# Optimization experiments

Hardware: AMD Instinct MI355X
Metric: run time of the kernel (lower is better)

The kernel has to match this reference:

```python
import jax, jax.numpy as jnp
import numpy as np

N_NODES = 100000
N_EDGES = 1600000
D_IN = 128
D_HID = 128
SCALE = 1.8
EPS = 1e-12


def setup_inputs() -> dict:
    key = jax.random.key(0)
    ks = jax.random.split(key, 7)
    x = jax.random.normal(ks[0], (N_NODES, D_IN), dtype=jnp.float32)
    W1 = jax.random.normal(ks[1], (D_HID, D_IN), dtype=jnp.float32) * 0.05
    b1 = jax.random.normal(ks[2], (D_HID,), dtype=jnp.float32) * 0.05
    W2 = jax.random.normal(ks[3], (D_HID, D_HID), dtype=jnp.float32) * 0.05
    b2 = jax.random.normal(ks[4], (D_HID,), dtype=jnp.float32) * 0.05
    src = jax.random.randint(ks[5], (N_EDGES,), 0, N_NODES, dtype=jnp.int64 if jax.config.jax_enable_x64 else jnp.int32)
    dst = jax.random.randint(ks[6], (N_EDGES,), 0, N_NODES, dtype=jnp.int64 if jax.config.jax_enable_x64 else jnp.int32)
    return {"x": x, "W1": W1, "b1": b1, "W2": W2, "b2": b2, "src": src, "dst": dst}


def reference(x, W1, b1, W2, b2, src, dst):
    N = x.shape[0]
    ones = jnp.ones((src.shape[0],), dtype=x.dtype)
    # GraphConv norm='both' degree normalizers (clamped to >=1 as in DGL)
    deg_out = jnp.maximum(jnp.zeros((N,), x.dtype).at[src].add(ones), 1.0)
    deg_in = jnp.maximum(jnp.zeros((N,), x.dtype).at[dst].add(ones), 1.0)
    norm_out = jax.lax.rsqrt(deg_out)[:, None]  # [N,1]
    norm_in = jax.lax.rsqrt(deg_in)[:, None]    # [N,1]

    def layer(h, W, b):
        # torch.nn.Linear: h @ W.T + b
        h = jnp.einsum('nd,kd->nk', h, W) + b
        # F.normalize(h, dim=1) * 1.8
        nrm = jnp.sqrt(jnp.sum(h * h, axis=1, keepdims=True))
        h = h / jnp.maximum(nrm, EPS) * SCALE
        # GraphConv (weight=False, bias=False, norm='both'):
        # D_out^{-1/2} -> sparse aggregate -> D_in^{-1/2}
        h = h * norm_out
        agg = jax.ops.segment_sum(h[src], dst, num_segments=N)
        return agg * norm_in

    h = layer(x, W1, b1)
    h = layer(h, W2, b2)
    return h
```

## Files before the change

kernel.cpp:

```cpp
#include <hip/hip_runtime.h>
#include <cstdint>
#include <cstddef>

#define D 128
#define NSCALE 1.8f
#define NEPS 1e-12f
#define EPB 8192
#define NLO 512
#define SCAP 9216
#define SRCB 23
#define SRCM 0x7FFFFF

typedef __attribute__((ext_vector_type(8))) short bf16x8;
typedef __attribute__((ext_vector_type(4))) float f32x4;

__device__ __forceinline__ ushort bf16_rtn(float f) {
    uint32_t u = __float_as_uint(f);
    u = u + 0x7FFFu + ((u >> 16) & 1u);
    return (ushort)(u >> 16);
}

__device__ __forceinline__ float blo(uint32_t u) { return __uint_as_float(u << 16); }
__device__ __forceinline__ float bhi(uint32_t u) { return __uint_as_float(u & 0xFFFF0000u); }

__global__ __launch_bounds__(256) void hist_high_kernel(const int* __restrict__ src,
                                                        const int* __restrict__ dst,
                                                        int* __restrict__ Hd,
                                                        int* __restrict__ Hs, int ne) {
    __shared__ int hd[256], hs[256];
    int t = threadIdx.x, b = blockIdx.x;
    hd[t] = 0; hs[t] = 0;
    __syncthreads();
    int base = b * EPB, end = min(ne, base + EPB);
    for (int i = base + t; i < end; i += 256) {
        atomicAdd(&hd[dst[i] >> 9], 1);
        atomicAdd(&hs[src[i] >> 9], 1);
    }
    __syncthreads();
    Hd[b * 256 + t] = hd[t];
    Hs[b * 256 + t] = hs[t];
}

__global__ __launch_bounds__(256) void scan_cols_kernel(int* __restrict__ Hd,
                                                        int* __restrict__ Hs,
                                                        int* __restrict__ total_d,
                                                        int* __restrict__ total_s, int nbk) {
    __shared__ int s[256];
    int* H = blockIdx.y ? Hs : Hd;
    int* tot = blockIdx.y ? total_s : total_d;
    int v = blockIdx.x, t = threadIdx.x;
    int val = (t < nbk) ? H[t * 256 + v] : 0;
    s[t] = val;
    __syncthreads();
    #pragma unroll
    for (int off = 1; off < 256; off <<= 1) {
        int u = (t >= off) ? s[t - off] : 0;
        __syncthreads();
        s[t] += u;
        __syncthreads();
    }
    if (t < nbk) H[t * 256 + v] = s[t] - val;
    if (t == nbk - 1) tot[v] = s[t];
}

__global__ __launch_bounds__(256) void scan_tot_kernel(const int* __restrict__ total_d,
                                                       const int* __restrict__ total_s,
                                                       int* __restrict__ Bd,
                                                       int* __restrict__ Bs, int hb) {
    __shared__ int s[256];
    const int* tot = blockIdx.x ? total_s : total_d;
    int* B = blockIdx.x ? Bs : Bd;
    int t = threadIdx.x;
    int val = (t < hb) ? tot[t] : 0;
    s[t] = val;
    __syncthreads();
    #pragma unroll
    for (int off = 1; off < 256; off <<= 1) {
        int u = (t >= off) ? s[t - off] : 0;
        __syncthreads();
        s[t] += u;
        __syncthreads();
    }
    if (t <= hb) B[t] = s[t] - val;
}

__global__ __launch_bounds__(256) void scatter_high_kernel(const int* __restrict__ src,
                                                           const int* __restrict__ dst,
                                                           const int* __restrict__ Hd,
                                                           const int* __restrict__ Hs,
                                                           const int* __restrict__ Bd,
                                                           const int* __restrict__ Bs,
                                                           uint32_t* __restrict__ spack,
                                                           ushort* __restrict__ ss_low,
                                                           int ne, int hb) {
    __shared__ int cur_d[256], cur_s[256];
    int t = threadIdx.x, b = blockIdx.x;
    if (t < hb) {
        cur_d[t] = Bd[t] + Hd[b * 256 + t];
        cur_s[t] = Bs[t] + Hs[b * 256 + t];
    }
    __syncthreads();
    int base = b * EPB, end = min(ne, base + EPB);
    for (int i = base + t; i < end; i += 256) {
        int d = dst[i], s = src[i];
        int pd = atomicAdd(&cur_d[d >> 9], 1);
        spack[pd] = ((uint32_t)(d & (NLO - 1)) << SRCB) | (uint32_t)s;
        int ps = atomicAdd(&cur_s[s >> 9], 1);
        ss_low[ps] = (ushort)(s & (NLO - 1));
    }
}

__global__ __launch_bounds__(512) void bucket_sort_kernel(const uint32_t* __restrict__ spack,
                                                          const int* __restrict__ Bd,
                                                          int* __restrict__ offs,
                                                          int* __restrict__ cnt_dst,
                                                          float* __restrict__ norm_in,
                                                          int* __restrict__ ssrc, int N) {
    __shared__ int h[NLO], sc[NLO], cur[NLO];
    __shared__ int stage[SCAP];
    int t = threadIdx.x, v = blockIdx.x;
    int beg = Bd[v], end = Bd[v + 1];
    int m = end - beg;
    h[t] = 0;
    __syncthreads();
    for (int i = beg + t; i < end; i += 512) atomicAdd(&h[spack[i] >> SRCB], 1);
    __syncthreads();
    int cnt = h[t];
    sc[t] = cnt;
    __syncthreads();
    #pragma unroll
    for (int off = 1; off < NLO; off <<= 1) {
        int u = (t >= off) ? sc[t - off] : 0;
        __syncthreads();
        sc[t] += u;
        __syncthreads();
    }
    int excl = sc[t] - cnt;
    int g = (v << 9) + t;
    if (g < N) {
        offs[g] = beg + excl;
        cnt_dst[g] = cnt;
        norm_in[g] = rsqrtf((float)max(cnt, 1));
    }
    if (m <= SCAP) {
        cur[t] = excl;
        __syncthreads();
        for (int i = beg + t; i < end; i += 512) {
            uint32_t p = spack[i];
            int pos = atomicAdd(&cur[p >> SRCB], 1);
            stage[pos] = (int)(p & SRCM);
        }
        __syncthreads();
        for (int j = t; j < m; j += 512) ssrc[beg + j] = stage[j];
    } else {
        cur[t] = beg + excl;
        __syncthreads();
        for (int i = beg + t; i < end; i += 512) {
            uint32_t p = spack[i];
            int pos = atomicAdd(&cur[p >> SRCB], 1);
            ssrc[pos] = (int)(p & SRCM);
        }
    }
}

__global__ __launch_bounds__(512) void bucket_hist_kernel(const ushort* __restrict__ ss_low,
                                                          const int* __restrict__ Bs,
                                                          float* __restrict__ norm_out, int N) {
    __shared__ int h[NLO];
    int t = threadIdx.x, v = blockIdx.x;
    int beg = Bs[v], end = Bs[v + 1];
    h[t] = 0;
    __syncthreads();
    for (int i = beg + t; i < end; i += 512) atomicAdd(&h[(int)ss_low[i]], 1);
    __syncthreads();
    int g = (v << 9) + t;
    if (g < N) norm_out[g] = rsqrtf((float)max(h[t], 1));
}

__global__ __launch_bounds__(256) void mlp_mfma_kernel(const float* __restrict__ X,
                                                       const float* __restrict__ W,
                                                       const float* __restrict__ b,
                                                       const float* __restrict__ post,
                                                       ushort* __restrict__ Abuf, int N) {
    __shared__ ushort Wf[128 * 128];

    const int t = threadIdx.x;
    const int wave = t >> 6;
    const int lane = t & 63;
    const int q = lane >> 4;
    const int l16 = lane & 15;

    if (blockIdx.x == 0 && t < 16) {
        ((uint4*)(Abuf + (size_t)N * D))[t] = make_uint4(0u, 0u, 0u, 0u);
    }

    #pragma unroll
    for (int it = 0; it < 8; ++it) {
        int f = t + 256 * it;
        int j = f >> 8;
        int p = (f >> 6) & 3;
        int ln = f & 63;
        int n = 16 * j + (ln & 15);
        int k0 = 32 * p + 8 * (ln >> 4);
        const float* srcp = W + n * D + k0;
        float4 a0 = *(const float4*)(srcp);
        float4 a1 = *(const float4*)(srcp + 4);
        bf16x8 v;
        v[0] = (short)bf16_rtn(a0.x); v[1] = (short)bf16_rtn(a0.y);
        v[2] = (short)bf16_rtn(a0.z); v[3] = (short)bf16_rtn(a0.w);
        v[4] = (short)bf16_rtn(a1.x); v[5] = (short)bf16_rtn(a1.y);
        v[6] = (short)bf16_rtn(a1.z); v[7] = (short)bf16_rtn(a1.w);
        ((bf16x8*)Wf)[f] = v;
    }

    const int r0 = blockIdx.x * 128 + wave * 32;
    bf16x8 ahi[2][4], alo[2][4];
    #pragma unroll
    for (int rt = 0; rt < 2; ++rt) {
        int row = r0 + rt * 16 + l16;
        bool ok = (row < N);
        const float* xr = X + (size_t)(ok ? row : 0) * D;
        #pragma unroll
        for (int p = 0; p < 4; ++p) {
            int k0 = 32 * p + 8 * q;
            float4 a0 = ok ? *(const float4*)(xr + k0)     : make_float4(0, 0, 0, 0);
            float4 a1 = ok ? *(const float4*)(xr + k0 + 4) : make_float4(0, 0, 0, 0);
            float fv[8] = {a0.x, a0.y, a0.z, a0.w, a1.x, a1.y, a1.z, a1.w};
            bf16x8 h, l;
            #pragma unroll
            for (int e = 0; e < 8; ++e) {
                uint32_t u = __float_as_uint(fv[e]);
                h[e] = (short)(u >> 16);
                float hf = __uint_as_float(u & 0xFFFF0000u);
                l[e] = (short)(__float_as_uint(fv[e] - hf) >> 16);
            }
            ahi[rt][p] = h;
            alo[rt][p] = l;
        }
    }

    __syncthreads();

    f32x4 acc[2][8];
    #pragma unroll
    for (int rt = 0; rt < 2; ++rt)
        #pragma unroll
        for (int j = 0; j < 8; ++j) acc[rt][j] = (f32x4){0.f, 0.f, 0.f, 0.f};

    #pragma unroll
    for (int j = 0; j < 8; ++j) {
        #pragma unroll
        for (int p = 0; p < 4; ++p) {
            bf16x8 bb = ((bf16x8*)Wf)[(j * 4 + p) * 64 + lane];
            acc[0][j] = __builtin_amdgcn_mfma_f32_16x16x32_bf16(ahi[0][p], bb, acc[0][j], 0, 0, 0);
            acc[0][j] = __builtin_amdgcn_mfma_f32_16x16x32_bf16(alo[0][p], bb, acc[0][j], 0, 0, 0);
            acc[1][j] = __builtin_amdgcn_mfma_f32_16x16x32_bf16(ahi[1][p], bb, acc[1][j], 0, 0, 0);
            acc[1][j] = __builtin_amdgcn_mfma_f32_16x16x32_bf16(alo[1][p], bb, acc[1][j], 0, 0, 0);
        }
    }

    float bias[8];
    #pragma unroll
    for (int j = 0; j < 8; ++j) bias[j] = b[16 * j + l16];

    #pragma unroll
    for (int rt = 0; rt < 2; ++rt) {
        float ss[4] = {0.f, 0.f, 0.f, 0.f};
        #pragma unroll
        for (int j = 0; j < 8; ++j)
            #pragma unroll
            for (int r = 0; r < 4; ++r) {
                float v = acc[rt][j][r] + bias[j];
                acc[rt][j][r] = v;
                ss[r] += v * v;
            }
        #pragma unroll
        for (int m = 1; m <= 8; m <<= 1)
            #pragma unroll
            for (int r = 0; r < 4; ++r) ss[r] += __shfl_xor(ss[r], m);

        #pragma unroll
        for (int r = 0; r < 4; ++r) {
            int row = r0 + rt * 16 + 4 * q + r;
            if (row < N) {
                float f = NSCALE / fmaxf(sqrtf(ss[r]), NEPS) * post[row];
                #pragma unroll
                for (int j = 0; j < 8; ++j)
                    Abuf[(size_t)row * D + 16 * j + l16] = bf16_rtn(acc[rt][j][r] * f);
            }
        }
    }
}

__global__ __launch_bounds__(256) void agg_kernel(const ushort* __restrict__ A,
                                                  const int* __restrict__ sorted_src,
                                                  const int* __restrict__ offs,
                                                  const int* __restrict__ cnt,
                                                  const float* __restrict__ norm_in,
                                                  float* __restrict__ out, int N) {
    int wave = threadIdx.x >> 6;
    int n0 = (blockIdx.x * 4 + wave) * 2;
    if (n0 >= N) return;
    int lane = threadIdx.x & 63;
    int g = lane >> 4;
    int c = lane & 15;
    const ushort* Ac = A + c * 8;

    int n1 = n0 + 1;
    int beg0 = offs[n0], len0 = cnt[n0];
    int beg1 = 0, len1 = 0;
    if (n1 < N) { beg1 = offs[n1]; len1 = cnt[n1]; }
    int last0 = beg0 + len0 - 1;
    int last1 = beg1 + len1 - 1;

    float a0[8] = {0.f, 0.f, 0.f, 0.f, 0.f, 0.f, 0.f, 0.f};
    float a1[8] = {0.f, 0.f, 0.f, 0.f, 0.f, 0.f, 0.f, 0.f};

    int mx = max(len0, len1);
    for (int i = 0; i < mx; i += 16) {
        int idx[8];
        #pragma unroll
        for (int k = 0; k < 4; ++k) {
            int e = beg0 + i + g + 4 * k;
            int cl = max(min(e, last0), 0);
            idx[k] = sorted_src[cl];
            if (e > last0) idx[k] = N;
        }
        #pragma unroll
        for (int k = 0; k < 4; ++k) {
            int e = beg1 + i + g + 4 * k;
            int cl = max(min(e, last1), 0);
            idx[4 + k] = sorted_src[cl];
            if (e > last1) idx[4 + k] = N;
        }
        uint4 w[8];
        #pragma unroll
        for (int k = 0; k < 8; ++k) w[k] = *(const uint4*)(Ac + (size_t)idx[k] * D);
        #pragma unroll
        for (int k = 0; k < 4; ++k) {
            a0[0] += blo(w[k].x); a0[1] += bhi(w[k].x);
            a0[2] += blo(w[k].y); a0[3] += bhi(w[k].y);
            a0[4] += blo(w[k].z); a0[5] += bhi(w[k].z);
            a0[6] += blo(w[k].w); a0[7] += bhi(w[k].w);
        }
        #pragma unroll
        for (int k = 4; k < 8; ++k) {
            a1[0] += blo(w[k].x); a1[1] += bhi(w[k].x);
            a1[2] += blo(w[k].y); a1[3] += bhi(w[k].y);
            a1[4] += blo(w[k].z); a1[5] += bhi(w[k].z);
            a1[6] += blo(w[k].w); a1[7] += bhi(w[k].w);
        }
    }

    #pragma unroll
    for (int e = 0; e < 8; ++e) {
        a0[e] += __shfl_xor(a0[e], 16);
        a0[e] += __shfl_xor(a0[e], 32);
        a1[e] += __shfl_xor(a1[e], 16);
        a1[e] += __shfl_xor(a1[e], 32);
    }

    if (g == 0) {
        float sc0 = norm_in[n0];
        float* op0 = out + (size_t)n0 * D + c * 8;
        *(float4*)(op0)     = make_float4(a0[0] * sc0, a0[1] * sc0, a0[2] * sc0, a0[3] * sc0);
        *(float4*)(op0 + 4) = make_float4(a0[4] * sc0, a0[5] * sc0, a0[6] * sc0, a0[7] * sc0);
        if (n1 < N) {
            float sc1 = norm_in[n1];
            float* op1 = out + (size_t)n1 * D + c * 8;
            *(float4*)(op1)     = make_float4(a1[0] * sc1, a1[1] * sc1, a1[2] * sc1, a1[3] * sc1);
            *(float4*)(op1 + 4) = make_float4(a1[4] * sc1, a1[5] * sc1, a1[6] * sc1, a1[7] * sc1);
        }
    }
}


extern "C" void kernel_launch(void* const* d_in, const int* in_sizes, int n_in,
                              void* d_out, int out_size, void* d_ws, size_t ws_size,
                              hipStream_t stream) {
    const float* x  = (const float*)d_in[0];
    const float* W1 = (const float*)d_in[1];
    const float* b1 = (const float*)d_in[2];
    const float* W2 = (const float*)d_in[3];
    const float* b2 = (const float*)d_in[4];
    const int* src  = (const int*)d_in[5];
    const int* dst  = (const int*)d_in[6];
    float* out = (float*)d_out;

    const int N  = in_sizes[0] / D;
    const int NE = in_sizes[5];
    const int NBK = (NE + EPB - 1) / EPB;
    const int HB  = (N + NLO - 1) / NLO;

    char* w = (char*)d_ws;
    auto take = [&](size_t bytes) { char* p = w; w += (bytes + 255) & ~(size_t)255; return p; };
    int*      Hd       = (int*)take((size_t)NBK * 256 * 4);
    int*      Hs       = (int*)take((size_t)NBK * 256 * 4);
    int*      total_d  = (int*)take(256 * 4);
    int*      total_s  = (int*)take(256 * 4);
    int*      Bd       = (int*)take((size_t)(HB + 1) * 4);
    int*      Bs       = (int*)take((size_t)(HB + 1) * 4);
    uint32_t* spack    = (uint32_t*)take((size_t)NE * 4);
    ushort*   ss_low   = (ushort*)take((size_t)NE * 2);
    int*      ssrc     = (int*)take((size_t)NE * 4);
    int*      offs     = (int*)take((size_t)N * 4);
    int*      cnt_dst  = (int*)take((size_t)N * 4);
    float*    norm_in  = (float*)take((size_t)N * 4);
    float*    norm_out = (float*)take((size_t)N * 4);
    ushort*   Abuf     = (ushort*)take((size_t)(N + 1) * D * 2);

    hist_high_kernel<<<NBK, 256, 0, stream>>>(src, dst, Hd, Hs, NE);
    scan_cols_kernel<<<dim3(HB, 2), 256, 0, stream>>>(Hd, Hs, total_d, total_s, NBK);
    scan_tot_kernel<<<2, 256, 0, stream>>>(total_d, total_s, Bd, Bs, HB);
    scatter_high_kernel<<<NBK, 256, 0, stream>>>(src, dst, Hd, Hs, Bd, Bs,
                                                 spack, ss_low, NE, HB);
    bucket_sort_kernel<<<HB, 512, 0, stream>>>(spack, Bd, offs, cnt_dst, norm_in, ssrc, N);
    bucket_hist_kernel<<<HB, 512, 0, stream>>>(ss_low, Bs, norm_out, N);

    const int mlp_blocks = (N + 127) / 128;
    const int agg_blocks = (N + 7) / 8;

    mlp_mfma_kernel<<<mlp_blocks, 256, 0, stream>>>(x, W1, b1, norm_out, Abuf, N);
    agg_kernel<<<agg_blocks, 256, 0, stream>>>(Abuf, ssrc, offs, cnt_dst, norm_in, out, N);

    mlp_mfma_kernel<<<mlp_blocks, 256, 0, stream>>>(out, W2, b2, norm_out, Abuf, N);
    agg_kernel<<<agg_blocks, 256, 0, stream>>>(Abuf, ssrc, offs, cnt_dst, norm_in, out, N);
}
```

Baseline: 335.5 us.

## Shrink edge chunks, transpose histogram layout, and widen bucket kernels to 1024 threads

Edges per histogram/scatter block drop from 8192 to 2048, so those kernels launch about four times as many blocks (782 instead of 196). The per-block histograms are stored transposed with a padded stride, and each scan thread handles four consecutive entries, so column scans read contiguous memory and can cover up to 1024 blocks. The bucket sort and bucket histogram kernels move to 1024 threads per block, with the extra threads used only in the edge loops. The cost is a larger histogram buffer and more scan work per thread.

```diff
diff --git a/kernel.cpp b/kernel.cpp
--- a/kernel.cpp
+++ b/kernel.cpp
@@ -5,7 +5,8 @@
 #define D 128
 #define NSCALE 1.8f
 #define NEPS 1e-12f
-#define EPB 8192
+#define EPB 2048
+#define NBPAD 784
 #define NLO 512
 #define SCAP 9216
 #define SRCB 23
@@ -37,8 +38,8 @@
         atomicAdd(&hs[src[i] >> 9], 1);
     }
     __syncthreads();
-    Hd[b * 256 + t] = hd[t];
-    Hs[b * 256 + t] = hs[t];
+    Hd[t * NBPAD + b] = hd[t];
+    Hs[t * NBPAD + b] = hs[t];
 }
 
 __global__ __launch_bounds__(256) void scan_cols_kernel(int* __restrict__ Hd,
@@ -49,8 +50,13 @@
     int* H = blockIdx.y ? Hs : Hd;
     int* tot = blockIdx.y ? total_s : total_d;
     int v = blockIdx.x, t = threadIdx.x;
-    int val = (t < nbk) ? H[t * 256 + v] : 0;
-    s[t] = val;
+    int base = v * NBPAD + 4 * t;
+    int a0 = (4 * t + 0 < nbk) ? H[base + 0] : 0;
+    int a1 = (4 * t + 1 < nbk) ? H[base + 1] : 0;
+    int a2 = (4 * t + 2 < nbk) ? H[base + 2] : 0;
+    int a3 = (4 * t + 3 < nbk) ? H[base + 3] : 0;
+    int sum = a0 + a1 + a2 + a3;
+    s[t] = sum;
     __syncthreads();
     #pragma unroll
     for (int off = 1; off < 256; off <<= 1) {
@@ -59,8 +65,12 @@
         s[t] += u;
         __syncthreads();
     }
-    if (t < nbk) H[t * 256 + v] = s[t] - val;
-    if (t == nbk - 1) tot[v] = s[t];
+    int excl = s[t] - sum;
+    if (4 * t + 0 < nbk) H[base + 0] = excl;
+    if (4 * t + 1 < nbk) H[base + 1] = excl + a0;
+    if (4 * t + 2 < nbk) H[base + 2] = excl + a0 + a1;
+    if (4 * t + 3 < nbk) H[base + 3] = excl + a0 + a1 + a2;
+    if (t == 255) tot[v] = s[255];
 }
 
 __global__ __launch_bounds__(256) void scan_tot_kernel(const int* __restrict__ total_d,
@@ -96,8 +106,8 @@
     __shared__ int cur_d[256], cur_s[256];
     int t = threadIdx.x, b = blockIdx.x;
     if (t < hb) {
-        cur_d[t] = Bd[t] + Hd[b * 256 + t];
-        cur_s[t] = Bs[t] + Hs[b * 256 + t];
+        cur_d[t] = Bd[t] + Hd[t * NBPAD + b];
+        cur_s[t] = Bs[t] + Hs[t * NBPAD + b];
     }
     __syncthreads();
     int base = b * EPB, end = min(ne, base + EPB);
@@ -110,52 +120,52 @@
     }
 }
 
-__global__ __launch_bounds__(512) void bucket_sort_kernel(const uint32_t* __restrict__ spack,
-                                                          const int* __restrict__ Bd,
-                                                          int* __restrict__ offs,
-                                                          int* __restrict__ cnt_dst,
-                                                          float* __restrict__ norm_in,
-                                                          int* __restrict__ ssrc, int N) {
+__global__ __launch_bounds__(1024) void bucket_sort_kernel(const uint32_t* __restrict__ spack,
+                                                           const int* __restrict__ Bd,
+                                                           int* __restrict__ offs,
+                                                           int* __restrict__ cnt_dst,
+                                                           float* __restrict__ norm_in,
+                                                           int* __restrict__ ssrc, int N) {
     __shared__ int h[NLO], sc[NLO], cur[NLO];
     __shared__ int stage[SCAP];
     int t = threadIdx.x, v = blockIdx.x;
     int beg = Bd[v], end = Bd[v + 1];
     int m = end - beg;
-    h[t] = 0;
-    __syncthreads();
-    for (int i = beg + t; i < end; i += 512) atomicAdd(&h[spack[i] >> SRCB], 1);
-    __syncthreads();
-    int cnt = h[t];
-    sc[t] = cnt;
+    if (t < NLO) h[t] = 0;
+    __syncthreads();
+    for (int i = beg + t; i < end; i += 1024) atomicAdd(&h[spack[i] >> SRCB], 1);
+    __syncthreads();
+    int cnt = 0;
+    if (t < NLO) { cnt = h[t]; sc[t] = cnt; }
     __syncthreads();
     #pragma unroll
     for (int off = 1; off < NLO; off <<= 1) {
-        int u = (t >= off) ? sc[t - off] : 0;
-        __syncthreads();
-        sc[t] += u;
-        __syncthreads();
-    }
-    int excl = sc[t] - cnt;
+        int u = (t >= off && t < NLO) ? sc[t - off] : 0;
+        __syncthreads();
+        if (t < NLO) sc[t] += u;
+        __syncthreads();
+    }
+    int excl = (t < NLO) ? (sc[t] - cnt) : 0;
     int g = (v << 9) + t;
-    if (g < N) {
+    if (t < NLO && g < N) {
         offs[g] = beg + excl;
         cnt_dst[g] = cnt;
         norm_in[g] = rsqrtf((float)max(cnt, 1));
     }
     if (m <= SCAP) {
-        cur[t] = excl;
-        __syncthreads();
-        for (int i = beg + t; i < end; i += 512) {
+        if (t < NLO) cur[t] = excl;
+        __syncthreads();
+        for (int i = beg + t; i < end; i += 1024) {
             uint32_t p = spack[i];
             int pos = atomicAdd(&cur[p >> SRCB], 1);
             stage[pos] = (int)(p & SRCM);
         }
         __syncthreads();
-        for (int j = t; j < m; j += 512) ssrc[beg + j] = stage[j];
+        for (int j = t; j < m; j += 1024) ssrc[beg + j] = stage[j];
     } else {
-        cur[t] = beg + excl;
-        __syncthreads();
-        for (int i = beg + t; i < end; i += 512) {
+        if (t < NLO) cur[t] = beg + excl;
+        __syncthreads();
+        for (int i = beg + t; i < end; i += 1024) {
             uint32_t p = spack[i];
             int pos = atomicAdd(&cur[p >> SRCB], 1);
             ssrc[pos] = (int)(p & SRCM);
@@ -163,18 +173,18 @@
     }
 }
 
-__global__ __launch_bounds__(512) void bucket_hist_kernel(const ushort* __restrict__ ss_low,
-                                                          const int* __restrict__ Bs,
-                                                          float* __restrict__ norm_out, int N) {
+__global__ __launch_bounds__(1024) void bucket_hist_kernel(const ushort* __restrict__ ss_low,
+                                                           const int* __restrict__ Bs,
+                                                           float* __restrict__ norm_out, int N) {
     __shared__ int h[NLO];
     int t = threadIdx.x, v = blockIdx.x;
     int beg = Bs[v], end = Bs[v + 1];
-    h[t] = 0;
-    __syncthreads();
-    for (int i = beg + t; i < end; i += 512) atomicAdd(&h[(int)ss_low[i]], 1);
+    if (t < NLO) h[t] = 0;
+    __syncthreads();
+    for (int i = beg + t; i < end; i += 1024) atomicAdd(&h[(int)ss_low[i]], 1);
     __syncthreads();
     int g = (v << 9) + t;
-    if (g < N) norm_out[g] = rsqrtf((float)max(h[t], 1));
+    if (t < NLO && g < N) norm_out[g] = rsqrtf((float)max(h[t], 1));
 }
 
 __global__ __launch_bounds__(256) void mlp_mfma_kernel(const float* __restrict__ X,
@@ -394,8 +404,8 @@
 
     char* w = (char*)d_ws;
     auto take = [&](size_t bytes) { char* p = w; w += (bytes + 255) & ~(size_t)255; return p; };
-    int*      Hd       = (int*)take((size_t)NBK * 256 * 4);
-    int*      Hs       = (int*)take((size_t)NBK * 256 * 4);
+    int*      Hd       = (int*)take((size_t)256 * NBPAD * 4);
+    int*      Hs       = (int*)take((size_t)256 * NBPAD * 4);
     int*      total_d  = (int*)take(256 * 4);
     int*      total_s  = (int*)take(256 * 4);
     int*      Bd       = (int*)take((size_t)(HB + 1) * 4);
@@ -414,8 +424,8 @@
     scan_tot_kernel<<<2, 256, 0, stream>>>(total_d, total_s, Bd, Bs, HB);
     scatter_high_kernel<<<NBK, 256, 0, stream>>>(src, dst, Hd, Hs, Bd, Bs,
                                                  spack, ss_low, NE, HB);
-    bucket_sort_kernel<<<HB, 512, 0, stream>>>(spack, Bd, offs, cnt_dst, norm_in, ssrc, N);
-    bucket_hist_kernel<<<HB, 512, 0, stream>>>(ss_low, Bs, norm_out, N);
+    bucket_sort_kernel<<<HB, 1024, 0, stream>>>(spack, Bd, offs, cnt_dst, norm_in, ssrc, N);
+    bucket_hist_kernel<<<HB, 1024, 0, stream>>>(ss_low, Bs, norm_out, N);
 
     const int mlp_blocks = (N + 127) / 128;
     const int agg_blocks = (N + 7) / 8;
```

After: 333.2 us. About the same (-0.7%).
